# Kernel optimization log

Measured on AMD Instinct MI355X. Metric: run time of the kernel, lower is better.

The kernel has to match this reference:

```python
import jax, jax.numpy as jnp
import numpy as np

TAU_MIN, TAU_MAX = 0.02, 2.0
LN_EPS = 1e-5


def setup_inputs() -> dict:
    key = jax.random.key(0)
    ks = jax.random.split(key, 7)
    N, H = 16777216, 16
    neigh3 = jax.random.normal(ks[0], (N, 3), dtype=jnp.float32)
    # LayerNorm(3) affine params
    ln_w = jnp.ones((3,), dtype=jnp.float32)
    ln_b = jnp.zeros((3,), dtype=jnp.float32)
    # Linear(3, 16): torch default init U(-1/sqrt(3), 1/sqrt(3))
    lim1 = 1.0 / np.sqrt(3.0)
    w1 = jax.random.uniform(ks[1], (H, 3), minval=-lim1, maxval=lim1, dtype=jnp.float32)
    b1 = jax.random.uniform(ks[2], (H,), minval=-lim1, maxval=lim1, dtype=jnp.float32)
    # Linear(16, 3)
    lim2 = 1.0 / np.sqrt(float(H))
    w2 = jax.random.uniform(ks[3], (3, H), minval=-lim2, maxval=lim2, dtype=jnp.float32)
    b2 = jax.random.uniform(ks[4], (3,), minval=-lim2, maxval=lim2, dtype=jnp.float32)
    log_tau = jnp.log(jnp.asarray(0.2, dtype=jnp.float32))
    return {"neigh3": neigh3, "ln_w": ln_w, "ln_b": ln_b,
            "w1": w1, "b1": b1, "w2": w2, "b2": b2, "log_tau": log_tau}


def _layernorm(x, w, b):
    mu = jnp.mean(x, axis=-1, keepdims=True)
    var = jnp.mean(jnp.square(x - mu), axis=-1, keepdims=True)
    return (x - mu) * jax.lax.rsqrt(var + LN_EPS) * w + b


def reference(neigh3, ln_w, ln_b, w1, b1, w2, b2, log_tau):
    tau = jnp.clip(jnp.exp(log_tau), TAU_MIN, TAU_MAX)
    # soft-min via -tau * logsumexp(-x/tau) over last dim (size 3)
    best_vals = -tau * jax.nn.logsumexp(-neigh3 / tau, axis=-1)   # [N]
    feats = -jnp.abs(neigh3 - best_vals[..., None])               # [N,3]
    h = _layernorm(feats, ln_w, ln_b)                             # [N,3]
    h = jax.nn.relu(jnp.einsum('nc,hc->nh', h, w1) + b1)          # [N,16]
    logits = jnp.einsum('nh,ch->nc', h, w2) + b2                  # [N,3]
    weights = jax.nn.softmax(logits, axis=-1)
    return jnp.sum(neigh3 * weights, axis=-1)                     # [N]
```

## Files before the change

kernel.cpp:

```cpp
#include <hip/hip_runtime.h>
#include <math.h>

typedef float vf4 __attribute__((ext_vector_type(4)));

#define LN_EPS 1e-5f
#define NBINS  1024


__global__ void nn2_lut_setup(const float* __restrict__ lnw, const float* __restrict__ lnb,
                              const float* __restrict__ w1,  const float* __restrict__ b1,
                              const float* __restrict__ w2,  const float* __restrict__ b2,
                              float* __restrict__ ws)
{
    int i = blockIdx.x * blockDim.x + threadIdx.x;
    if (i >= NBINS) return;
    float v  = (float)i * (4.0f / NBINS) - 1.0f;
    float dd = (v <= 1.0f) ? v : (2.0f - v);
    float Pm = 1.0f - fabsf(dd);
    float P  = (v <= 1.0f) ? Pm : -Pm;
    float Q  = dd;
    float n = rsqrtf(P * P + Q * Q);
    float p = 1.7320508075688772f * P * n;
    float q = 1.7320508075688772f * Q * n;
    const float is2 = 0.7071067811865476f;
    const float is6 = 0.4082482904638631f;
    float t0 =  p * is2 + q * is6;
    float t1 = -p * is2 + q * is6;
    float t2 = -2.0f * q * is6;
    float h0 = t0 * lnw[0] + lnb[0];
    float h1 = t1 * lnw[1] + lnb[1];
    float h2 = t2 * lnw[2] + lnb[2];
    float l0 = b2[0], l1 = b2[1], l2 = b2[2];
    for (int j = 0; j < 16; ++j) {
        float a = fmaf(w1[3*j], h0, fmaf(w1[3*j+1], h1, fmaf(w1[3*j+2], h2, b1[j])));
        a = fmaxf(a, 0.0f);
        l0 = fmaf(w2[j],    a, l0);
        l1 = fmaf(w2[16+j], a, l1);
        l2 = fmaf(w2[32+j], a, l2);
    }
    float m  = fmaxf(l0, fmaxf(l1, l2));
    float e0 = expf(l0 - m), e1 = expf(l1 - m), e2 = expf(l2 - m);
    float r  = 1.0f / (e0 + e1 + e2);
    ws[i]           = e0 * r;
    ws[NBINS + i]   = e1 * r;
    ws[2*NBINS + i] = e2 * r;
}

__device__ __forceinline__ float row_out(float x0, float x1, float x2,
                                         const float* __restrict__ lut)
{
    float P   = (x1 - x0) * 1.7320508075688772f;
    float Q   = fmaf(2.0f, x2, -(x0 + x1));
    float den = fabsf(P) + fabsf(Q) + 1e-20f;
    float dd  = Q * __builtin_amdgcn_rcpf(den);
    float v   = (P >= 0.0f) ? dd : (2.0f - dd);
    float u   = fmaf(v, 256.0f, 256.0f);
    int   iu  = (int)u;
    float f   = u - (float)iu;
    int i0 = iu & (NBINS - 1);
    int i1 = (iu + 1) & (NBINS - 1);
    float a0 = lut[i0],           b0 = lut[i1];
    float a1 = lut[NBINS + i0],   b1 = lut[NBINS + i1];
    float a2 = lut[2*NBINS + i0], b2 = lut[2*NBINS + i1];
    float w0 = fmaf(f, b0 - a0, a0);
    float w1 = fmaf(f, b1 - a1, a1);
    float w2 = fmaf(f, b2 - a2, a2);
    return fmaf(x0, w0, fmaf(x1, w1, x2 * w2));
}

__global__ __launch_bounds__(256) void nn2_lut_main(
    const float* __restrict__ x, const float* __restrict__ ws,
    float* __restrict__ out, int nrows, int pthreads)
{
    __shared__ float lut[3 * NBINS];
    int tid = threadIdx.x;
#pragma unroll
    for (int k = 0; k < (3 * NBINS) / 256; ++k)
        lut[tid + 256 * k] = ws[tid + 256 * k];
    __syncthreads();

    long long T = ((long long)nrows + 3) >> 2;
    const vf4* x4 = reinterpret_cast<const vf4*>(x);
    vf4* out4 = reinterpret_cast<vf4*>(out);

    for (long long grp = (long long)blockIdx.x * blockDim.x + tid; grp < T;
         grp += pthreads) {
        long long base = grp * 4;
        float X[4][3];
        bool full = (base + 4 <= nrows);
        if (full) {
            vf4 va = x4[grp*3 + 0], vb = x4[grp*3 + 1], vc = x4[grp*3 + 2];
            X[0][0]=va.x; X[0][1]=va.y; X[0][2]=va.z;
            X[1][0]=va.w; X[1][1]=vb.x; X[1][2]=vb.y;
            X[2][0]=vb.z; X[2][1]=vb.w; X[2][2]=vc.x;
            X[3][0]=vc.y; X[3][1]=vc.z; X[3][2]=vc.w;
        } else {
#pragma unroll
            for (int r = 0; r < 4; ++r) {
                long long rr = (base + r < nrows) ? base + r : (long long)nrows - 1;
                X[r][0]=x[rr*3]; X[r][1]=x[rr*3+1]; X[r][2]=x[rr*3+2];
            }
        }
        float O[4];
#pragma unroll
        for (int r = 0; r < 4; ++r)
            O[r] = row_out(X[r][0], X[r][1], X[r][2], lut);

        if (full) {
            vf4 o; o.x=O[0]; o.y=O[1]; o.z=O[2]; o.w=O[3];
            __builtin_nontemporal_store(o, &out4[grp]);
        } else {
            for (int r = 0; r < 4 && base + r < nrows; ++r) out[base + r] = O[r];
        }
    }
}

__global__ __launch_bounds__(256) void nn2_fallback(
    const float* __restrict__ x,
    const float* __restrict__ lnw_g, const float* __restrict__ lnb_g,
    const float* __restrict__ w1_g,  const float* __restrict__ b1_g,
    const float* __restrict__ w2_g,  const float* __restrict__ b2_g,
    float* __restrict__ out, int nrows)
{
    int g = blockIdx.x * blockDim.x + threadIdx.x;
    long long base = (long long)g * 4;
    if (base >= nrows) return;
    const float lw0 = lnw_g[0], lw1 = lnw_g[1], lw2 = lnw_g[2];
    const float lb0 = lnb_g[0], lb1 = lnb_g[1], lb2 = lnb_g[2];
    float X[4][3];
    if (base + 4 <= nrows) {
        const float4* x4 = reinterpret_cast<const float4*>(x) + (long long)g * 3;
        float4 va = x4[0], vb = x4[1], vc = x4[2];
        X[0][0]=va.x; X[0][1]=va.y; X[0][2]=va.z;
        X[1][0]=va.w; X[1][1]=vb.x; X[1][2]=vb.y;
        X[2][0]=vb.z; X[2][1]=vb.w; X[2][2]=vc.x;
        X[3][0]=vc.y; X[3][1]=vc.z; X[3][2]=vc.w;
    } else {
        for (int r = 0; r < 4; ++r) {
            long long rr = (base + r < nrows) ? base + r : (long long)nrows - 1;
            X[r][0]=x[rr*3]; X[r][1]=x[rr*3+1]; X[r][2]=x[rr*3+2];
        }
    }
    float H[4][3];
#pragma unroll
    for (int r = 0; r < 4; ++r) {
        float x0=X[r][0], x1=X[r][1], x2=X[r][2];
        float mu=(x0+x1+x2)*(1.0f/3.0f);
        float d0=mu-x0, d1=mu-x1, d2=mu-x2;
        float rs=__builtin_amdgcn_rsqf(fmaf(fmaf(d0,d0,fmaf(d1,d1,d2*d2)),1.0f/3.0f,LN_EPS));
        H[r][0]=fmaf(d0*rs,lw0,lb0); H[r][1]=fmaf(d1*rs,lw1,lb1); H[r][2]=fmaf(d2*rs,lw2,lb2);
    }
    float L[4][3];
    { const float b20=b2_g[0],b21=b2_g[1],b22=b2_g[2];
#pragma unroll
      for (int r=0;r<4;++r){L[r][0]=b20;L[r][1]=b21;L[r][2]=b22;} }
#pragma unroll
    for (int j = 0; j < 16; ++j) {
        const float a0=w1_g[3*j],a1=w1_g[3*j+1],a2=w1_g[3*j+2],bj=b1_g[j];
        const float u0=w2_g[j],u1=w2_g[16+j],u2=w2_g[32+j];
#pragma unroll
        for (int r=0;r<4;++r){
            float hj=fmaf(H[r][2],a2,fmaf(H[r][1],a1,fmaf(H[r][0],a0,bj)));
            hj=fmaxf(hj,0.0f);
            L[r][0]=fmaf(hj,u0,L[r][0]); L[r][1]=fmaf(hj,u1,L[r][1]); L[r][2]=fmaf(hj,u2,L[r][2]);
        }
    }
    float O[4];
#pragma unroll
    for (int r=0;r<4;++r){
        float l0=L[r][0],l1=L[r][1],l2=L[r][2];
        float lm=fmaxf(l0,fmaxf(l1,l2));
        float s0=__expf(l0-lm),s1=__expf(l1-lm),s2=__expf(l2-lm);
        float rc=__builtin_amdgcn_rcpf(s0+s1+s2);
        O[r]=fmaf(X[r][0],s0,fmaf(X[r][1],s1,X[r][2]*s2))*rc;
    }
    if (base + 4 <= nrows) {
        float4 o; o.x=O[0];o.y=O[1];o.z=O[2];o.w=O[3];
        reinterpret_cast<float4*>(out)[g] = o;
    } else {
        for (int r = 0; r < 4 && base + r < nrows; ++r) out[base + r] = O[r];
    }
}

extern "C" void kernel_launch(void* const* d_in, const int* in_sizes, int n_in,
                              void* d_out, int out_size, void* d_ws, size_t ws_size,
                              hipStream_t stream) {
    const float* x    = (const float*)d_in[0];
    const float* lnw  = (const float*)d_in[1];
    const float* lnb  = (const float*)d_in[2];
    const float* w1   = (const float*)d_in[3];
    const float* b1   = (const float*)d_in[4];
    const float* w2   = (const float*)d_in[5];
    const float* b2   = (const float*)d_in[6];
    float* out = (float*)d_out;
    int nrows = out_size;

    if (ws_size >= (size_t)(3 * NBINS) * sizeof(float)) {
        float* ws = (float*)d_ws;
        nn2_lut_setup<<<NBINS / 256, 256, 0, stream>>>(lnw, lnb, w1, b1, w2, b2, ws);
        long long T = ((long long)nrows + 3) / 4;
        int grid = 2048;
        long long need = (T + 255) / 256;
        if (need < grid) grid = (int)need;
        int pthreads = grid * 256;
        nn2_lut_main<<<grid, 256, 0, stream>>>(x, ws, out, nrows, pthreads);
    } else {
        int ngroups = (nrows + 3) / 4;
        int grid    = (ngroups + 255) / 256;
        nn2_fallback<<<grid, 256, 0, stream>>>(x, lnw, lnb, w1, b1, w2, b2, out, nrows);
    }
}
```

Before: 49.20 us.

## Pack softmax LUT as fp16 pairs and software-pipeline input loads

The lookup table now holds two fp16 weights packed into one 32-bit word per node. The third weight is recovered from the weights summing to one, and two extra wrap nodes remove the index masking. The grid-stride loop now prefetches the next group's three vector loads before computing the current group, so memory latency overlaps with compute. This cuts LDS traffic and load count per row, at the cost of fp16 rounding in the interpolated weights and higher register pressure from the double-buffered inputs.

```diff
diff --git a/kernel.cpp b/kernel.cpp
--- a/kernel.cpp
+++ b/kernel.cpp
@@ -1,20 +1,24 @@
 #include <hip/hip_runtime.h>
+#include <hip/hip_fp16.h>
 #include <math.h>
 
 typedef float vf4 __attribute__((ext_vector_type(4)));
+typedef unsigned int u32;
 
 #define LN_EPS 1e-5f
 #define NBINS  1024
+#define NLUT   (NBINS + 2)
 
 
 __global__ void nn2_lut_setup(const float* __restrict__ lnw, const float* __restrict__ lnb,
                               const float* __restrict__ w1,  const float* __restrict__ b1,
                               const float* __restrict__ w2,  const float* __restrict__ b2,
-                              float* __restrict__ ws)
+                              u32* __restrict__ ws)
 {
     int i = blockIdx.x * blockDim.x + threadIdx.x;
-    if (i >= NBINS) return;
-    float v  = (float)i * (4.0f / NBINS) - 1.0f;
+    if (i >= NLUT) return;
+    int node = i & (NBINS - 1);
+    float v  = (float)node * (4.0f / NBINS) - 1.0f;
     float dd = (v <= 1.0f) ? v : (2.0f - v);
     float Pm = 1.0f - fabsf(dd);
     float P  = (v <= 1.0f) ? Pm : -Pm;
@@ -41,13 +45,14 @@
     float m  = fmaxf(l0, fmaxf(l1, l2));
     float e0 = expf(l0 - m), e1 = expf(l1 - m), e2 = expf(l2 - m);
     float r  = 1.0f / (e0 + e1 + e2);
-    ws[i]           = e0 * r;
-    ws[NBINS + i]   = e1 * r;
-    ws[2*NBINS + i] = e2 * r;
+    float W0 = e0 * r, W1 = e1 * r;
+    u32 pk = ((u32)__half_as_ushort(__float2half_rn(W1)) << 16)
+           |  (u32)__half_as_ushort(__float2half_rn(W0));
+    ws[i] = pk;
 }
 
 __device__ __forceinline__ float row_out(float x0, float x1, float x2,
-                                         const float* __restrict__ lut)
+                                         const u32* lut)
 {
     float P   = (x1 - x0) * 1.7320508075688772f;
     float Q   = fmaf(2.0f, x2, -(x0 + x1));
@@ -56,62 +61,62 @@
     float v   = (P >= 0.0f) ? dd : (2.0f - dd);
     float u   = fmaf(v, 256.0f, 256.0f);
     int   iu  = (int)u;
+    iu = iu < 0 ? 0 : (iu > NBINS ? NBINS : iu);
     float f   = u - (float)iu;
-    int i0 = iu & (NBINS - 1);
-    int i1 = (iu + 1) & (NBINS - 1);
-    float a0 = lut[i0],           b0 = lut[i1];
-    float a1 = lut[NBINS + i0],   b1 = lut[NBINS + i1];
-    float a2 = lut[2*NBINS + i0], b2 = lut[2*NBINS + i1];
+    u32 n0 = lut[iu];
+    u32 n1 = lut[iu + 1];
+    float a0 = __half2float(__ushort_as_half((unsigned short)(n0 & 0xffffu)));
+    float a1 = __half2float(__ushort_as_half((unsigned short)(n0 >> 16)));
+    float b0 = __half2float(__ushort_as_half((unsigned short)(n1 & 0xffffu)));
+    float b1 = __half2float(__ushort_as_half((unsigned short)(n1 >> 16)));
     float w0 = fmaf(f, b0 - a0, a0);
     float w1 = fmaf(f, b1 - a1, a1);
-    float w2 = fmaf(f, b2 - a2, a2);
-    return fmaf(x0, w0, fmaf(x1, w1, x2 * w2));
+    return fmaf(w0, x0 - x2, fmaf(w1, x1 - x2, x2));
 }
 
 __global__ __launch_bounds__(256) void nn2_lut_main(
-    const float* __restrict__ x, const float* __restrict__ ws,
-    float* __restrict__ out, int nrows, int pthreads)
-{
-    __shared__ float lut[3 * NBINS];
+    const float* __restrict__ x, const u32* __restrict__ ws,
+    float* __restrict__ out, long long nrows, long long T, long long stride)
+{
+    __shared__ u32 lut[NLUT];
     int tid = threadIdx.x;
-#pragma unroll
-    for (int k = 0; k < (3 * NBINS) / 256; ++k)
-        lut[tid + 256 * k] = ws[tid + 256 * k];
+    for (int k = tid; k < NLUT; k += 256) lut[k] = ws[k];
     __syncthreads();
 
-    long long T = ((long long)nrows + 3) >> 2;
-    const vf4* x4 = reinterpret_cast<const vf4*>(x);
-    vf4* out4 = reinterpret_cast<vf4*>(out);
-
-    for (long long grp = (long long)blockIdx.x * blockDim.x + tid; grp < T;
-         grp += pthreads) {
-        long long base = grp * 4;
-        float X[4][3];
-        bool full = (base + 4 <= nrows);
+    const vf4* x4  = reinterpret_cast<const vf4*>(x);
+    vf4*       out4 = reinterpret_cast<vf4*>(out);
+
+    long long grp = (long long)blockIdx.x * 256 + tid;
+    if (grp >= T) return;
+
+    vf4 va, vb, vc;
+    bool full = (grp * 4 + 4 <= nrows);
+    if (full) { va = x4[grp*3]; vb = x4[grp*3 + 1]; vc = x4[grp*3 + 2]; }
+
+    while (true) {
+        long long nxt = grp + stride;
+        bool nhas = (nxt < T);
+        bool nfull = false;
+        vf4 na, nb, nc;
+        if (nhas) {
+            nfull = (nxt * 4 + 4 <= nrows);
+            if (nfull) { na = x4[nxt*3]; nb = x4[nxt*3 + 1]; nc = x4[nxt*3 + 2]; }
+        }
+
         if (full) {
-            vf4 va = x4[grp*3 + 0], vb = x4[grp*3 + 1], vc = x4[grp*3 + 2];
-            X[0][0]=va.x; X[0][1]=va.y; X[0][2]=va.z;
-            X[1][0]=va.w; X[1][1]=vb.x; X[1][2]=vb.y;
-            X[2][0]=vb.z; X[2][1]=vb.w; X[2][2]=vc.x;
-            X[3][0]=vc.y; X[3][1]=vc.z; X[3][2]=vc.w;
-        } else {
-#pragma unroll
-            for (int r = 0; r < 4; ++r) {
-                long long rr = (base + r < nrows) ? base + r : (long long)nrows - 1;
-                X[r][0]=x[rr*3]; X[r][1]=x[rr*3+1]; X[r][2]=x[rr*3+2];
-            }
-        }
-        float O[4];
-#pragma unroll
-        for (int r = 0; r < 4; ++r)
-            O[r] = row_out(X[r][0], X[r][1], X[r][2], lut);
-
-        if (full) {
-            vf4 o; o.x=O[0]; o.y=O[1]; o.z=O[2]; o.w=O[3];
+            vf4 o;
+            o.x = row_out(va.x, va.y, va.z, lut);
+            o.y = row_out(va.w, vb.x, vb.y, lut);
+            o.z = row_out(vb.z, vb.w, vc.x, lut);
+            o.w = row_out(vc.y, vc.z, vc.w, lut);
             __builtin_nontemporal_store(o, &out4[grp]);
         } else {
-            for (int r = 0; r < 4 && base + r < nrows; ++r) out[base + r] = O[r];
-        }
+            for (long long r = grp * 4; r < nrows; ++r)
+                out[r] = row_out(x[r*3], x[r*3 + 1], x[r*3 + 2], lut);
+        }
+
+        if (!nhas) break;
+        grp = nxt; full = nfull; va = na; vb = nb; vc = nc;
     }
 }
 
@@ -193,20 +198,19 @@
     const float* w2   = (const float*)d_in[5];
     const float* b2   = (const float*)d_in[6];
     float* out = (float*)d_out;
-    int nrows = out_size;
-
-    if (ws_size >= (size_t)(3 * NBINS) * sizeof(float)) {
-        float* ws = (float*)d_ws;
-        nn2_lut_setup<<<NBINS / 256, 256, 0, stream>>>(lnw, lnb, w1, b1, w2, b2, ws);
-        long long T = ((long long)nrows + 3) / 4;
-        int grid = 2048;
+    long long nrows = out_size;
+
+    if (ws_size >= (size_t)NLUT * sizeof(u32)) {
+        u32* ws = (u32*)d_ws;
+        nn2_lut_setup<<<(NLUT + 255) / 256, 256, 0, stream>>>(lnw, lnb, w1, b1, w2, b2, ws);
+        long long T = (nrows + 3) / 4;
         long long need = (T + 255) / 256;
-        if (need < grid) grid = (int)need;
-        int pthreads = grid * 256;
-        nn2_lut_main<<<grid, 256, 0, stream>>>(x, ws, out, nrows, pthreads);
+        int grid = (need < 2048) ? (int)need : 2048;
+        long long stride = (long long)grid * 256;
+        nn2_lut_main<<<grid, 256, 0, stream>>>(x, ws, out, nrows, T, stride);
     } else {
-        int ngroups = (nrows + 3) / 4;
-        int grid    = (ngroups + 255) / 256;
-        nn2_fallback<<<grid, 256, 0, stream>>>(x, lnw, lnb, w1, b1, w2, b2, out, nrows);
-    }
-}
+        long long ngroups = (nrows + 3) / 4;
+        int grid = (int)((ngroups + 255) / 256);
+        nn2_fallback<<<grid, 256, 0, stream>>>(x, lnw, lnb, w1, b1, w2, b2, out, (int)nrows);
+    }
+}
```

Result: no change. 50.06 us (+1.8%).
